# Performance work log

Measured on AMD Instinct MI355X. Metric: run time of the kernel, lower is better.

The kernel has to match this reference:

```python
import jax, jax.numpy as jnp
import numpy as np

B, A, F, D, C = 256, 128, 512, 6, 512  # batch, max_atoms, atom_features, max_degree, conv_width


def setup_inputs() -> dict:
    key = jax.random.key(0)
    k1, k2, k3, k4 = jax.random.split(key, 4)
    atoms = jax.random.normal(k1, (B, A, F), dtype=jnp.float32)
    # neighbour indices in [0, A); pad entries beyond each atom's degree with -1
    neigh = jax.random.randint(k2, (B, A, D), 0, A)
    deg = jax.random.randint(k3, (B, A, 1), 0, D)  # degrees in 0..D-1
    bonds = jnp.where(jnp.arange(D)[None, None, :] < deg, neigh, -1)
    # one Dense(conv_width) per degree: stacked kernels [D, F, C] and biases [D, C]
    W = jax.random.normal(k4, (D, F, C), dtype=jnp.float32) * 0.02
    b = jnp.zeros((D, C), dtype=jnp.float32)
    return {"atoms": atoms, "bonds": bonds, "W": W, "b": b}


def reference(atoms, bonds, W, b):
    d_max = bonds.shape[-1]
    # per-atom degree = count of non -1 neighbour slots  [B, A, 1]
    degrees = jnp.sum(bonds != -1, axis=-1, keepdims=True)
    # shift lookup by 1 so that padded (-1) neighbours index a zero row
    padded = jnp.pad(atoms, ((0, 0), (1, 1), (0, 0)))  # [B, A+2, F]
    idx = bonds + 1  # [B, A, D]
    # per-sample gather of neighbour features -> [B, A, D, F]
    neigh_feats = jax.vmap(lambda ref, i: ref[i])(padded, idx)
    summed = jnp.sum(neigh_feats, axis=2) + atoms  # [B, A, F]
    # apply all degree-specific dense layers, then mask-select by degree
    dense = jnp.einsum('baf,dfc->badc', summed, W) + b  # [B, A, D, C]
    masks = (degrees[..., None] == jnp.arange(d_max).reshape(1, 1, d_max, 1)).astype(dense.dtype)
    return jnp.sum(dense * masks, axis=2)  # [B, A, C]
```

## Files before the change

### kernel.cpp

```cpp
#include <hip/hip_runtime.h>
#include <hip/hip_bf16.h>


#define NB 256
#define NA 128
#define NF 512
#define ND 6
#define NC 512
#define NATOMS (NB * NA)

typedef __attribute__((ext_vector_type(8))) short frag8;
typedef __attribute__((ext_vector_type(4))) float f32x4;

static __device__ inline unsigned short f2bu(float f) {
    __hip_bfloat16 h = __float2bfloat16(f);
    return *reinterpret_cast<unsigned short*>(&h);
}
static __device__ inline unsigned int pack2(float a, float b) {
    return (unsigned int)f2bu(a) | ((unsigned int)f2bu(b) << 16);
}
static __device__ inline void async16(const void* g, void* l) {
    __builtin_amdgcn_global_load_lds(
        (const __attribute__((address_space(1))) void*)g,
        (__attribute__((address_space(3))) void*)l, 16, 0, 0);
}

__global__ void transpose_w(const float* __restrict__ W,
                            __hip_bfloat16* __restrict__ Wt) {
    __shared__ float t[32][33];
    const int d  = blockIdx.z;
    const int c0 = blockIdx.x * 32;
    const int f0 = blockIdx.y * 32;
    #pragma unroll
    for (int r = 0; r < 32; r += 8)
        t[threadIdx.y + r][threadIdx.x] =
            W[((size_t)(d * NF + f0 + threadIdx.y + r)) * NC + c0 + threadIdx.x];
    __syncthreads();
    #pragma unroll
    for (int r = 0; r < 32; r += 8)
        Wt[((size_t)(d * NC + c0 + threadIdx.y + r)) * NF + f0 + threadIdx.x] =
            __float2bfloat16(t[threadIdx.x][threadIdx.y + r]);
}

__global__ __launch_bounds__(256) void bucket_atoms(
    const int* __restrict__ bonds, int* __restrict__ counts,
    int* __restrict__ bucket) {
    __shared__ int lcnt[ND];
    __shared__ int lbase[ND];
    const int tid = threadIdx.x;
    if (tid < ND) lcnt[tid] = 0;
    __syncthreads();
    int deg[4], loc[4], gg[4];
    #pragma unroll
    for (int i = 0; i < 4; ++i) {
        int g = blockIdx.x * 1024 + i * 256 + tid;
        gg[i] = g;
        int dg = 0;
        #pragma unroll
        for (int j = 0; j < ND; ++j) dg += (bonds[g * ND + j] >= 0);
        deg[i] = dg;
        loc[i] = atomicAdd(&lcnt[dg], 1);
    }
    __syncthreads();
    if (tid < ND) lbase[tid] = atomicAdd(&counts[tid], lcnt[tid]);
    __syncthreads();
    #pragma unroll
    for (int i = 0; i < 4; ++i)
        bucket[deg[i] * NATOMS + lbase[deg[i]] + loc[i]] = gg[i];
}

__global__ __launch_bounds__(256) void sum_neigh(
    const float* __restrict__ atoms, const int* __restrict__ bonds,
    __hip_bfloat16* __restrict__ summed) {
    const int tid  = threadIdx.x;
    const int wave = tid >> 6;
    const int lane = tid & 63;
    const int g    = blockIdx.x * 4 + wave;
    const float4* a4 = (const float4*)atoms;

    int   nb[ND];
    float msk[ND];
    #pragma unroll
    for (int j = 0; j < ND; ++j) {
        int n = bonds[g * ND + j];
        msk[j] = (n >= 0) ? 1.0f : 0.0f;
        nb[j]  = (n >= 0) ? n : 0;
    }
    const int rowbase = g & ~(NA - 1);

    float4 s0 = a4[(size_t)g * 128 + lane];
    float4 s1 = a4[(size_t)g * 128 + 64 + lane];
    float4 v0[ND], v1[ND];
    #pragma unroll
    for (int j = 0; j < ND; ++j) {
        const size_t base = (size_t)(rowbase + nb[j]) * 128;
        v0[j] = a4[base + lane];
        v1[j] = a4[base + 64 + lane];
    }
    #pragma unroll
    for (int j = 0; j < ND; ++j) {
        s0.x = fmaf(v0[j].x, msk[j], s0.x); s0.y = fmaf(v0[j].y, msk[j], s0.y);
        s0.z = fmaf(v0[j].z, msk[j], s0.z); s0.w = fmaf(v0[j].w, msk[j], s0.w);
        s1.x = fmaf(v1[j].x, msk[j], s1.x); s1.y = fmaf(v1[j].y, msk[j], s1.y);
        s1.z = fmaf(v1[j].z, msk[j], s1.z); s1.w = fmaf(v1[j].w, msk[j], s1.w);
    }

    uint2 o0, o1;
    o0.x = pack2(s0.x, s0.y); o0.y = pack2(s0.z, s0.w);
    o1.x = pack2(s1.x, s1.y); o1.y = pack2(s1.z, s1.w);
    ((uint2*)summed)[(size_t)g * 128 + lane] = o0;
    ((uint2*)summed)[(size_t)g * 128 + 64 + lane] = o1;
}

__global__ __launch_bounds__(256, 4) void gemm_deg(
    const __hip_bfloat16* __restrict__ summed, const __hip_bfloat16* __restrict__ Wt,
    const float* __restrict__ bias, const int* __restrict__ counts,
    const int* __restrict__ bucket, float* __restrict__ out) {
    const int bx = blockIdx.x;
    const int d  = bx % ND;
    const int n0 = (bx / ND) * 128;
    const int Md = counts[d];
    const int m0 = blockIdx.y * 128;
    if (m0 >= Md) return;

    __shared__ __align__(16) __hip_bfloat16 sA[128 * 64];
    __shared__ __align__(16) __hip_bfloat16 sB[128 * 64];
    __shared__ int sRows[128];

    const int tid = threadIdx.x;
    if (tid < 128) {
        int r = m0 + tid;
        sRows[tid] = (r < Md) ? bucket[d * NATOMS + r] : -1;
    }
    __syncthreads();

    const int lane = tid & 63;
    const int w    = tid >> 6;
    const int srow = lane >> 3;
    const int seg  = lane & 7;

    const char* smB = (const char*)summed;
    const char* wtB = (const char*)Wt + (size_t)(d * NC + n0) * (NF * 2);
    size_t gA[4];
    int    rowc[4];
    #pragma unroll
    for (int c = 0; c < 4; ++c) {
        rowc[c] = w * 32 + c * 8 + srow;
        int q = sRows[rowc[c]];
        gA[c] = (size_t)((q < 0) ? 0 : q) * (NF * 2);
    }

    const int quad = lane >> 4, l16 = lane & 15;
    const int wy = w >> 1, wx = w & 1;

    f32x4 acc[4][4];
    #pragma unroll
    for (int i = 0; i < 4; ++i)
        #pragma unroll
        for (int j = 0; j < 4; ++j) acc[i][j] = (f32x4)0.0f;

    for (int kt = 0; kt < NF / 64; ++kt) {
        const int koff = kt * 128 + seg * 16;
        #pragma unroll
        for (int c = 0; c < 4; ++c) {
            async16(smB + gA[c] + koff, &sA[(w * 32 + c * 8) * 64]);
            async16(wtB + (size_t)rowc[c] * (NF * 2) + koff, &sB[(w * 32 + c * 8) * 64]);
        }
        __syncthreads();
        #pragma unroll
        for (int ks = 0; ks < 64; ks += 32) {
            frag8 aF[4], bF[4];
            #pragma unroll
            for (int i = 0; i < 4; ++i)
                aF[i] = *(const frag8*)&sA[(wy * 64 + i * 16 + l16) * 64 + ks + quad * 8];
            #pragma unroll
            for (int j = 0; j < 4; ++j)
                bF[j] = *(const frag8*)&sB[(wx * 64 + j * 16 + l16) * 64 + ks + quad * 8];
            #pragma unroll
            for (int i = 0; i < 4; ++i)
                #pragma unroll
                for (int j = 0; j < 4; ++j)
                    acc[i][j] = __builtin_amdgcn_mfma_f32_16x16x32_bf16(
                        aF[i], bF[j], acc[i][j], 0, 0, 0);
        }
        __syncthreads();
    }

    #pragma unroll
    for (int j = 0; j < 4; ++j) {
        const int n = n0 + wx * 64 + j * 16 + l16;
        const float bv = bias[d * NC + n];
        #pragma unroll
        for (int i = 0; i < 4; ++i) {
            #pragma unroll
            for (int r = 0; r < 4; ++r) {
                const int tr = wy * 64 + i * 16 + quad * 4 + r;
                const int g  = sRows[tr];
                if (g >= 0)
                    out[(size_t)g * NC + n] = acc[i][j][r] + bv;
            }
        }
    }
}

extern "C" void kernel_launch(void* const* d_in, const int* in_sizes, int n_in,
                              void* d_out, int out_size, void* d_ws, size_t ws_size,
                              hipStream_t stream) {
    const float* atoms = (const float*)d_in[0];
    const int*   bonds = (const int*)d_in[1];
    const float* W     = (const float*)d_in[2];
    const float* bias  = (const float*)d_in[3];
    float* out = (float*)d_out;

    char* ws = (char*)d_ws;
    int* counts = (int*)ws;
    int* bucket = (int*)(ws + 1024);
    __hip_bfloat16* Wt     = (__hip_bfloat16*)(ws + 1024 + 786432);
    __hip_bfloat16* summed = (__hip_bfloat16*)(ws + 1024 + 786432 + 3145728);

    hipMemsetAsync(counts, 0, 1024, stream);

    transpose_w<<<dim3(NC / 32, NF / 32, ND), dim3(32, 8), 0, stream>>>(W, Wt);

    bucket_atoms<<<NATOMS / 1024, 256, 0, stream>>>(bonds, counts, bucket);

    sum_neigh<<<NATOMS / 4, 256, 0, stream>>>(atoms, bonds, summed);

    gemm_deg<<<dim3(24, NATOMS / 128), 256, 0, stream>>>(
        summed, Wt, bias, counts, bucket, out);
}
```

Before: 184.2 us.

## Fuse prep kernels and double-buffer swizzled LDS in degree GEMM

Merges the weight transpose, degree bucketing and neighbour summation into one launch that dispatches work by block index range, removing two kernel launches and their serialization. The GEMM now double-buffers its LDS tiles, issuing the next k-tile's async loads before computing the current one. It also XOR-swizzles the 16-byte segments to avoid LDS bank conflicts on fragment reads. Occupancy is lowered to 2 blocks per CU because LDS use doubles. The neighbour-sum stores are widened to one 16-byte store per lane.

```diff
diff --git a/kernel.cpp b/kernel.cpp
--- a/kernel.cpp
+++ b/kernel.cpp
@@ -25,94 +25,96 @@
         (__attribute__((address_space(3))) void*)l, 16, 0, 0);
 }
 
-__global__ void transpose_w(const float* __restrict__ W,
-                            __hip_bfloat16* __restrict__ Wt) {
-    __shared__ float t[32][33];
-    const int d  = blockIdx.z;
-    const int c0 = blockIdx.x * 32;
-    const int f0 = blockIdx.y * 32;
-    #pragma unroll
-    for (int r = 0; r < 32; r += 8)
-        t[threadIdx.y + r][threadIdx.x] =
-            W[((size_t)(d * NF + f0 + threadIdx.y + r)) * NC + c0 + threadIdx.x];
-    __syncthreads();
-    #pragma unroll
-    for (int r = 0; r < 32; r += 8)
-        Wt[((size_t)(d * NC + c0 + threadIdx.y + r)) * NF + f0 + threadIdx.x] =
-            __float2bfloat16(t[threadIdx.x][threadIdx.y + r]);
-}
-
-__global__ __launch_bounds__(256) void bucket_atoms(
-    const int* __restrict__ bonds, int* __restrict__ counts,
+#define PREP_T 1536
+#define PREP_B (PREP_T + 32)
+#define PREP_S (PREP_B + NATOMS / 4)
+
+__global__ __launch_bounds__(256) void prep(
+    const float* __restrict__ atoms, const int* __restrict__ bonds,
+    const float* __restrict__ W, __hip_bfloat16* __restrict__ Wt,
+    __hip_bfloat16* __restrict__ summed, int* __restrict__ counts,
     int* __restrict__ bucket) {
-    __shared__ int lcnt[ND];
-    __shared__ int lbase[ND];
+    const int blk = blockIdx.x;
     const int tid = threadIdx.x;
-    if (tid < ND) lcnt[tid] = 0;
-    __syncthreads();
-    int deg[4], loc[4], gg[4];
-    #pragma unroll
-    for (int i = 0; i < 4; ++i) {
-        int g = blockIdx.x * 1024 + i * 256 + tid;
-        gg[i] = g;
-        int dg = 0;
-        #pragma unroll
-        for (int j = 0; j < ND; ++j) dg += (bonds[g * ND + j] >= 0);
-        deg[i] = dg;
-        loc[i] = atomicAdd(&lcnt[dg], 1);
-    }
-    __syncthreads();
-    if (tid < ND) lbase[tid] = atomicAdd(&counts[tid], lcnt[tid]);
-    __syncthreads();
-    #pragma unroll
-    for (int i = 0; i < 4; ++i)
-        bucket[deg[i] * NATOMS + lbase[deg[i]] + loc[i]] = gg[i];
-}
-
-__global__ __launch_bounds__(256) void sum_neigh(
-    const float* __restrict__ atoms, const int* __restrict__ bonds,
-    __hip_bfloat16* __restrict__ summed) {
-    const int tid  = threadIdx.x;
-    const int wave = tid >> 6;
-    const int lane = tid & 63;
-    const int g    = blockIdx.x * 4 + wave;
-    const float4* a4 = (const float4*)atoms;
-
-    int   nb[ND];
-    float msk[ND];
-    #pragma unroll
-    for (int j = 0; j < ND; ++j) {
-        int n = bonds[g * ND + j];
-        msk[j] = (n >= 0) ? 1.0f : 0.0f;
-        nb[j]  = (n >= 0) ? n : 0;
-    }
-    const int rowbase = g & ~(NA - 1);
-
-    float4 s0 = a4[(size_t)g * 128 + lane];
-    float4 s1 = a4[(size_t)g * 128 + 64 + lane];
-    float4 v0[ND], v1[ND];
-    #pragma unroll
-    for (int j = 0; j < ND; ++j) {
-        const size_t base = (size_t)(rowbase + nb[j]) * 128;
-        v0[j] = a4[base + lane];
-        v1[j] = a4[base + 64 + lane];
-    }
-    #pragma unroll
-    for (int j = 0; j < ND; ++j) {
-        s0.x = fmaf(v0[j].x, msk[j], s0.x); s0.y = fmaf(v0[j].y, msk[j], s0.y);
-        s0.z = fmaf(v0[j].z, msk[j], s0.z); s0.w = fmaf(v0[j].w, msk[j], s0.w);
-        s1.x = fmaf(v1[j].x, msk[j], s1.x); s1.y = fmaf(v1[j].y, msk[j], s1.y);
-        s1.z = fmaf(v1[j].z, msk[j], s1.z); s1.w = fmaf(v1[j].w, msk[j], s1.w);
-    }
-
-    uint2 o0, o1;
-    o0.x = pack2(s0.x, s0.y); o0.y = pack2(s0.z, s0.w);
-    o1.x = pack2(s1.x, s1.y); o1.y = pack2(s1.z, s1.w);
-    ((uint2*)summed)[(size_t)g * 128 + lane] = o0;
-    ((uint2*)summed)[(size_t)g * 128 + 64 + lane] = o1;
-}
-
-__global__ __launch_bounds__(256, 4) void gemm_deg(
+
+    if (blk < PREP_T) {
+        __shared__ float t[32][33];
+        const int tx = tid & 31, ty = tid >> 5;
+        const int d   = blk >> 8;
+        const int rem = blk & 255;
+        const int c0  = (rem & 15) * 32;
+        const int f0  = (rem >> 4) * 32;
+        #pragma unroll
+        for (int r = 0; r < 32; r += 8)
+            t[ty + r][tx] = W[((size_t)(d * NF + f0 + ty + r)) * NC + c0 + tx];
+        __syncthreads();
+        #pragma unroll
+        for (int r = 0; r < 32; r += 8)
+            Wt[((size_t)(d * NC + c0 + ty + r)) * NF + f0 + tx] =
+                __float2bfloat16(t[tx][ty + r]);
+    } else if (blk < PREP_B) {
+        __shared__ int lcnt[ND];
+        __shared__ int lbase[ND];
+        const int b = blk - PREP_T;
+        if (tid < ND) lcnt[tid] = 0;
+        __syncthreads();
+        int deg[4], loc[4], gg[4];
+        #pragma unroll
+        for (int i = 0; i < 4; ++i) {
+            int g = b * 1024 + i * 256 + tid;
+            gg[i] = g;
+            int dg = 0;
+            #pragma unroll
+            for (int j = 0; j < ND; ++j) dg += (bonds[g * ND + j] >= 0);
+            deg[i] = dg;
+            loc[i] = atomicAdd(&lcnt[dg], 1);
+        }
+        __syncthreads();
+        if (tid < ND) lbase[tid] = atomicAdd(&counts[tid], lcnt[tid]);
+        __syncthreads();
+        #pragma unroll
+        for (int i = 0; i < 4; ++i)
+            bucket[deg[i] * NATOMS + lbase[deg[i]] + loc[i]] = gg[i];
+    } else {
+        const int wave = tid >> 6;
+        const int lane = tid & 63;
+        const int g    = (blk - PREP_B) * 4 + wave;
+        const float4* a4 = (const float4*)atoms;
+
+        int   nb[ND];
+        float msk[ND];
+        #pragma unroll
+        for (int j = 0; j < ND; ++j) {
+            int n = bonds[g * ND + j];
+            msk[j] = (n >= 0) ? 1.0f : 0.0f;
+            nb[j]  = (n >= 0) ? n : 0;
+        }
+        const int rowbase = g & ~(NA - 1);
+
+        float4 s0 = a4[(size_t)g * 128 + 2 * lane];
+        float4 s1 = a4[(size_t)g * 128 + 2 * lane + 1];
+        float4 v0[ND], v1[ND];
+        #pragma unroll
+        for (int j = 0; j < ND; ++j) {
+            const size_t base = (size_t)(rowbase + nb[j]) * 128 + 2 * lane;
+            v0[j] = a4[base];
+            v1[j] = a4[base + 1];
+        }
+        #pragma unroll
+        for (int j = 0; j < ND; ++j) {
+            s0.x = fmaf(v0[j].x, msk[j], s0.x); s0.y = fmaf(v0[j].y, msk[j], s0.y);
+            s0.z = fmaf(v0[j].z, msk[j], s0.z); s0.w = fmaf(v0[j].w, msk[j], s0.w);
+            s1.x = fmaf(v1[j].x, msk[j], s1.x); s1.y = fmaf(v1[j].y, msk[j], s1.y);
+            s1.z = fmaf(v1[j].z, msk[j], s1.z); s1.w = fmaf(v1[j].w, msk[j], s1.w);
+        }
+        uint4 o;
+        o.x = pack2(s0.x, s0.y); o.y = pack2(s0.z, s0.w);
+        o.z = pack2(s1.x, s1.y); o.w = pack2(s1.z, s1.w);
+        ((uint4*)summed)[(size_t)g * 64 + lane] = o;
+    }
+}
+
+__global__ __launch_bounds__(256, 2) void gemm_deg(
     const __hip_bfloat16* __restrict__ summed, const __hip_bfloat16* __restrict__ Wt,
     const float* __restrict__ bias, const int* __restrict__ counts,
     const int* __restrict__ bucket, float* __restrict__ out) {
@@ -123,8 +125,8 @@
     const int m0 = blockIdx.y * 128;
     if (m0 >= Md) return;
 
-    __shared__ __align__(16) __hip_bfloat16 sA[128 * 64];
-    __shared__ __align__(16) __hip_bfloat16 sB[128 * 64];
+    __shared__ __align__(16) __hip_bfloat16 sA[2][128 * 64];
+    __shared__ __align__(16) __hip_bfloat16 sB[2][128 * 64];
     __shared__ int sRows[128];
 
     const int tid = threadIdx.x;
@@ -137,7 +139,8 @@
     const int lane = tid & 63;
     const int w    = tid >> 6;
     const int srow = lane >> 3;
-    const int seg  = lane & 7;
+    const int slot = lane & 7;
+    const int sseg = slot ^ srow;
 
     const char* smB = (const char*)summed;
     const char* wtB = (const char*)Wt + (size_t)(d * NC + n0) * (NF * 2);
@@ -159,23 +162,38 @@
         #pragma unroll
         for (int j = 0; j < 4; ++j) acc[i][j] = (f32x4)0.0f;
 
-    for (int kt = 0; kt < NF / 64; ++kt) {
-        const int koff = kt * 128 + seg * 16;
-        #pragma unroll
-        for (int c = 0; c < 4; ++c) {
-            async16(smB + gA[c] + koff, &sA[(w * 32 + c * 8) * 64]);
-            async16(wtB + (size_t)rowc[c] * (NF * 2) + koff, &sB[(w * 32 + c * 8) * 64]);
-        }
-        __syncthreads();
-        #pragma unroll
-        for (int ks = 0; ks < 64; ks += 32) {
+    #define STAGE(kt, p)                                                        \
+        {                                                                       \
+            const int koff = (kt) * 128 + sseg * 16;                            \
+            _Pragma("unroll")                                                   \
+            for (int c = 0; c < 4; ++c) {                                       \
+                async16(smB + gA[c] + koff, &sA[p][(w * 32 + c * 8) * 64]);     \
+                async16(wtB + (size_t)rowc[c] * (NF * 2) + koff,                \
+                        &sB[p][(w * 32 + c * 8) * 64]);                         \
+            }                                                                   \
+        }
+
+    STAGE(0, 0)
+    #pragma unroll
+    for (int kt = 0; kt < 8; ++kt) {
+        const int p = kt & 1;
+        __syncthreads();
+        if (kt < 7) STAGE(kt + 1, 1 - p)
+        #pragma unroll
+        for (int ks = 0; ks < 2; ++ks) {
             frag8 aF[4], bF[4];
             #pragma unroll
-            for (int i = 0; i < 4; ++i)
-                aF[i] = *(const frag8*)&sA[(wy * 64 + i * 16 + l16) * 64 + ks + quad * 8];
-            #pragma unroll
-            for (int j = 0; j < 4; ++j)
-                bF[j] = *(const frag8*)&sB[(wx * 64 + j * 16 + l16) * 64 + ks + quad * 8];
+            for (int i = 0; i < 4; ++i) {
+                const int R = wy * 64 + i * 16 + l16;
+                const int s = (quad + 4 * ks) ^ (R & 7);
+                aF[i] = *(const frag8*)&sA[p][R * 64 + s * 8];
+            }
+            #pragma unroll
+            for (int j = 0; j < 4; ++j) {
+                const int R = wx * 64 + j * 16 + l16;
+                const int s = (quad + 4 * ks) ^ (R & 7);
+                bF[j] = *(const frag8*)&sB[p][R * 64 + s * 8];
+            }
             #pragma unroll
             for (int i = 0; i < 4; ++i)
                 #pragma unroll
@@ -183,8 +201,8 @@
                     acc[i][j] = __builtin_amdgcn_mfma_f32_16x16x32_bf16(
                         aF[i], bF[j], acc[i][j], 0, 0, 0);
         }
-        __syncthreads();
-    }
+    }
+    #undef STAGE
 
     #pragma unroll
     for (int j = 0; j < 4; ++j) {
@@ -220,11 +238,7 @@
 
     hipMemsetAsync(counts, 0, 1024, stream);
 
-    transpose_w<<<dim3(NC / 32, NF / 32, ND), dim3(32, 8), 0, stream>>>(W, Wt);
-
-    bucket_atoms<<<NATOMS / 1024, 256, 0, stream>>>(bonds, counts, bucket);
-
-    sum_neigh<<<NATOMS / 4, 256, 0, stream>>>(atoms, bonds, summed);
+    prep<<<PREP_S, 256, 0, stream>>>(atoms, bonds, W, Wt, summed, counts, bucket);
 
     gemm_deg<<<dim3(24, NATOMS / 128), 256, 0, stream>>>(
         summed, Wt, bias, counts, bucket, out);
```

Measured after the change: 191.8 us. 4.1% more time.
